# Optimization experiments

Hardware: AMD Instinct MI355X
Metric: run time of the kernel (lower is better)

## Reference

```python
import jax, jax.numpy as jnp
import numpy as np

N_NODES = 100000
N_EDGES = 1600000
IN_F = 128
OUT_F = 32


def setup_inputs() -> dict:
    key = jax.random.key(0)
    k1, k2, k3, k4, k5 = jax.random.split(key, 5)
    x = jax.random.normal(k1, (N_NODES, IN_F), dtype=jnp.float32)
    edge_row = jax.random.randint(k2, (N_EDGES,), 0, N_NODES, dtype=jnp.int64 if jax.config.jax_enable_x64 else jnp.int32)
    edge_col = jax.random.randint(k3, (N_EDGES,), 0, N_NODES, dtype=jnp.int64 if jax.config.jax_enable_x64 else jnp.int32)
    edge_val = jax.random.uniform(k4, (N_EDGES,), dtype=jnp.float32)
    # Xavier-normal init like nn.init.xavier_normal_
    std = float(np.sqrt(2.0 / (IN_F + OUT_F)))
    weight = jax.random.normal(k5, (IN_F, OUT_F), dtype=jnp.float32) * std
    bias = jnp.zeros((OUT_F,), dtype=jnp.float32)
    return {"x": x, "edge_row": edge_row, "edge_col": edge_col,
            "edge_val": edge_val, "weight": weight, "bias": bias}


def reference(x, edge_row, edge_col, edge_val, weight, bias):
    # support = x @ W  (dense GEMM)
    support = x @ weight  # [N, out]
    # output = adj @ support, adj in COO form: out[row] += val * support[col]
    gathered = support[edge_col] * edge_val[:, None]  # [E, out]
    output = jax.ops.segment_sum(gathered, edge_row, num_segments=N_NODES)
    return output + bias
```

## Files before the change

### kernel.cpp

```cpp
#include <hip/hip_runtime.h>
#include <hip/hip_bf16.h>

#define N_NODES 100000
#define N_EDGES 1600000
#define IN_F 128
#define OUT_F 32

#define NBK 782
#define CAP 2816
#define CAPG 2432
#define TILE_A 4096
#define NWG_A 391
#define NWG_G 98
#define OVCAP 4096

typedef float v4f __attribute__((ext_vector_type(4)));
typedef short bf16x8 __attribute__((ext_vector_type(8)));
typedef float f32x4 __attribute__((ext_vector_type(4)));

__device__ inline unsigned short f2bf(float f) {
  unsigned u = __float_as_uint(f);
  return (unsigned short)((u + 0x7FFFu + ((u >> 16) & 1u)) >> 16);
}
__device__ inline float bf2f(unsigned short h) {
  return __uint_as_float(((unsigned)h) << 16);
}
__device__ inline unsigned pk2(float lo, float hi) {
  return (unsigned)f2bf(lo) | ((unsigned)f2bf(hi) << 16);
}

__global__ __launch_bounds__(1024) void gcn_fused_kernel(
    const float* __restrict__ x, const float* __restrict__ w,
    unsigned short* __restrict__ sup, const int* __restrict__ erow,
    const int* __restrict__ ecol, const float* __restrict__ eval,
    int* __restrict__ cursor, int* __restrict__ ovcnt, int4* __restrict__ ov,
    int2* __restrict__ bedges) {
  __shared__ int2 stage[TILE_A];
  __shared__ int dstg[TILE_A];
  __shared__ int h[NBK];
  __shared__ int lstart[NBK];
  __shared__ int gbase[NBK];
  __shared__ int lcur[NBK];
  const int t = threadIdx.x;

  if (blockIdx.x < NWG_G) {
    const int wid = t >> 6;
    const int lane = t & 63;
    const int lr = lane & 15;
    const int lg = lane >> 4;
    const int wrow0 = blockIdx.x * 1024 + wid * 64;

    bf16x8 bfrag[2][4];
    #pragma unroll
    for (int nt = 0; nt < 2; ++nt) {
      #pragma unroll
      for (int kk = 0; kk < 4; ++kk) {
        const int c = nt * 16 + lr;
        const int k0 = kk * 32 + lg * 8;
        union { unsigned u[4]; bf16x8 v; } bf;
        #pragma unroll
        for (int d = 0; d < 4; ++d)
          bf.u[d] = pk2(w[(k0 + 2 * d) * OUT_F + c],
                        w[(k0 + 2 * d + 1) * OUT_F + c]);
        bfrag[nt][kk] = bf.v;
      }
    }

    f32x4 acc[4][2];
    #pragma unroll
    for (int m = 0; m < 4; ++m) { acc[m][0] = 0.f; acc[m][1] = 0.f; }

    #pragma unroll
    for (int m = 0; m < 4; ++m) {
      const int row = wrow0 + m * 16 + lr;
      const int rl = (row < N_NODES) ? row : (N_NODES - 1);
      const float* xr = x + (size_t)rl * IN_F;
      #pragma unroll
      for (int kk = 0; kk < 4; ++kk) {
        const v4f p0 = *(const v4f*)(xr + kk * 32 + lg * 8);
        const v4f p1 = *(const v4f*)(xr + kk * 32 + lg * 8 + 4);
        union { unsigned u[4]; bf16x8 v; } af;
        af.u[0] = pk2(p0.x, p0.y);
        af.u[1] = pk2(p0.z, p0.w);
        af.u[2] = pk2(p1.x, p1.y);
        af.u[3] = pk2(p1.z, p1.w);
        acc[m][0] = __builtin_amdgcn_mfma_f32_16x16x32_bf16(af.v, bfrag[0][kk], acc[m][0], 0, 0, 0);
        acc[m][1] = __builtin_amdgcn_mfma_f32_16x16x32_bf16(af.v, bfrag[1][kk], acc[m][1], 0, 0, 0);
      }
    }
    #pragma unroll
    for (int m = 0; m < 4; ++m) {
      #pragma unroll
      for (int i = 0; i < 4; ++i) {
        const int r = wrow0 + m * 16 + lg * 4 + i;
        if (r < N_NODES) {
          sup[((size_t)r << 5) + lr] = f2bf(acc[m][0][i]);
          sup[((size_t)r << 5) + 16 + lr] = f2bf(acc[m][1][i]);
        }
      }
    }
  } else {
    const int base = (blockIdx.x - NWG_G) * TILE_A;
    const int tot = min(TILE_A, N_EDGES - base);
    for (int i = t; i < NBK; i += 1024) { h[i] = 0; lcur[i] = 0; }
    __syncthreads();

    int rowv[4], colv[4];
    float valv[4];
    #pragma unroll
    for (int i = 0; i < 4; ++i) {
      const int e = base + i * 1024 + t;
      if (e < N_EDGES) {
        rowv[i] = erow[e]; colv[i] = ecol[e]; valv[i] = eval[e];
        atomicAdd(&h[rowv[i] >> 7], 1);
      } else rowv[i] = -1;
    }
    __syncthreads();

    if (t < 64) {
      const int b0 = t * 13;
      int vals[13];
      int s = 0;
      #pragma unroll
      for (int i = 0; i < 13; ++i) {
        const int b = b0 + i;
        vals[i] = (b < NBK) ? h[b] : 0;
        s += vals[i];
      }
      int ssum = s;
      #pragma unroll
      for (int off = 1; off < 64; off <<= 1) {
        const int up = __shfl_up(ssum, off, 64);
        if (t >= off) ssum += up;
      }
      int excl = ssum - s;
      #pragma unroll
      for (int i = 0; i < 13; ++i) {
        const int b = b0 + i;
        if (b < NBK) { lstart[b] = excl; excl += vals[i]; }
      }
    }
    if (t < NBK) {
      const int c = h[t];
      gbase[t] = c ? atomicAdd(&cursor[t], c) : 0;
    }
    __syncthreads();

    #pragma unroll
    for (int i = 0; i < 4; ++i) {
      if (rowv[i] >= 0) {
        const int r = rowv[i];
        const int b = r >> 7;
        const int k = atomicAdd(&lcur[b], 1);
        const int idx = lstart[b] + k;
        const int lo = colv[i] | ((r & 127) << 17);
        const int hi = __float_as_int(valv[i]);
        stage[idx] = make_int2(lo, hi);
        const int dst = gbase[b] + k;
        if (dst < CAP) {
          dstg[idx] = b * CAP + dst;
        } else {
          dstg[idx] = -1;
          const int o = atomicAdd(ovcnt, 1);
          if (o < OVCAP) ov[o] = make_int4(b, lo, hi, 0);
        }
      }
    }
    __syncthreads();

    for (int j = t; j < tot; j += 1024) {
      const int d = dstg[j];
      if (d >= 0) bedges[d] = stage[j];
    }
  }
}

__global__ __launch_bounds__(512) void gcn_gather_kernel(
    const unsigned short* __restrict__ sup, const int* __restrict__ cursor,
    const int2* __restrict__ bedges, const int* __restrict__ ovcnt,
    const int4* __restrict__ ov, const float* __restrict__ bias,
    float* __restrict__ out) {
  __shared__ int2 stage[CAPG];
  __shared__ int2 sorted[CAPG];
  __shared__ int hist[128];
  __shared__ int csr[129];
  __shared__ int cur[128];
  const int t = threadIdx.x;
  const int b = blockIdx.x;
  const int f = t & 31;
  const int g = t >> 5;
  const int ext = min(cursor[b], CAPG);
  const size_t bb = (size_t)b * CAP;
  float acc[8] = {0.f, 0.f, 0.f, 0.f, 0.f, 0.f, 0.f, 0.f};

  if (t < 128) hist[t] = 0;
  __syncthreads();
  for (int j = t; j < ext; j += 512) {
    const int2 ed = bedges[bb + j];
    stage[j] = ed;
    if (ed.y != 0) atomicAdd(&hist[(ed.x >> 17) & 127], 1);
  }
  __syncthreads();
  if (t < 64) {
    const int v0 = hist[2 * t];
    const int v1 = hist[2 * t + 1];
    int s = v0 + v1;
    #pragma unroll
    for (int off = 1; off < 64; off <<= 1) {
      const int up = __shfl_up(s, off, 64);
      if (t >= off) s += up;
    }
    const int excl = s - (v0 + v1);
    csr[2 * t] = excl;
    csr[2 * t + 1] = excl + v0;
    cur[2 * t] = excl;
    cur[2 * t + 1] = excl + v0;
    if (t == 63) csr[128] = s;
  }
  __syncthreads();
  for (int j = t; j < ext; j += 512) {
    const int2 ed = stage[j];
    if (ed.y != 0) {
      const int k = atomicAdd(&cur[(ed.x >> 17) & 127], 1);
      sorted[k] = ed;
    }
  }
  __syncthreads();

  #pragma unroll
  for (int rr = 0; rr < 8; ++rr) {
    const int lr = g * 8 + rr;
    const int e1 = csr[lr + 1];
    int e = csr[lr];
    for (; e + 8 <= e1; e += 8) {
      const int2 q0 = sorted[e],     q1 = sorted[e + 1];
      const int2 q2 = sorted[e + 2], q3 = sorted[e + 3];
      const int2 q4 = sorted[e + 4], q5 = sorted[e + 5];
      const int2 q6 = sorted[e + 6], q7 = sorted[e + 7];
      const float v0 = bf2f(sup[((size_t)(q0.x & 0x1FFFF) << 5) + f]);
      const float v1 = bf2f(sup[((size_t)(q1.x & 0x1FFFF) << 5) + f]);
      const float v2 = bf2f(sup[((size_t)(q2.x & 0x1FFFF) << 5) + f]);
      const float v3 = bf2f(sup[((size_t)(q3.x & 0x1FFFF) << 5) + f]);
      const float v4 = bf2f(sup[((size_t)(q4.x & 0x1FFFF) << 5) + f]);
      const float v5 = bf2f(sup[((size_t)(q5.x & 0x1FFFF) << 5) + f]);
      const float v6 = bf2f(sup[((size_t)(q6.x & 0x1FFFF) << 5) + f]);
      const float v7 = bf2f(sup[((size_t)(q7.x & 0x1FFFF) << 5) + f]);
      acc[rr] += __int_as_float(q0.y) * v0 + __int_as_float(q1.y) * v1 +
                 __int_as_float(q2.y) * v2 + __int_as_float(q3.y) * v3 +
                 __int_as_float(q4.y) * v4 + __int_as_float(q5.y) * v5 +
                 __int_as_float(q6.y) * v6 + __int_as_float(q7.y) * v7;
    }
    for (; e + 4 <= e1; e += 4) {
      const int2 q0 = sorted[e],     q1 = sorted[e + 1];
      const int2 q2 = sorted[e + 2], q3 = sorted[e + 3];
      const float v0 = bf2f(sup[((size_t)(q0.x & 0x1FFFF) << 5) + f]);
      const float v1 = bf2f(sup[((size_t)(q1.x & 0x1FFFF) << 5) + f]);
      const float v2 = bf2f(sup[((size_t)(q2.x & 0x1FFFF) << 5) + f]);
      const float v3 = bf2f(sup[((size_t)(q3.x & 0x1FFFF) << 5) + f]);
      acc[rr] += __int_as_float(q0.y) * v0 + __int_as_float(q1.y) * v1 +
                 __int_as_float(q2.y) * v2 + __int_as_float(q3.y) * v3;
    }
    for (; e < e1; ++e) {
      const int2 q = sorted[e];
      acc[rr] += __int_as_float(q.y) *
                 bf2f(sup[((size_t)(q.x & 0x1FFFF) << 5) + f]);
    }
  }

  const int on = min(*ovcnt, OVCAP);
  for (int i = 0; i < on; ++i) {
    const int4 q = ov[i];
    if (q.x == b) {
      const int lr = (q.y >> 17) & 127;
      if ((lr >> 3) == g)
        acc[lr & 7] += __int_as_float(q.z) *
                       bf2f(sup[((size_t)(q.y & 0x1FFFF) << 5) + f]);
    }
  }

  const int row0 = b << 7;
  const float bv = bias[f];
  #pragma unroll
  for (int rr = 0; rr < 8; ++rr) {
    const int row = row0 + g * 8 + rr;
    if (row < N_NODES) out[((size_t)row << 5) + f] = acc[rr] + bv;
  }
}

__global__ __launch_bounds__(256) void gcn_gemm_fb_kernel(
    const float* __restrict__ x, const float* __restrict__ w,
    unsigned short* __restrict__ sup) {
  __shared__ float wlds[IN_F][OUT_F];
  const int t = threadIdx.x;
  for (int i = t; i < 1024; i += 256)
    ((float4*)wlds)[i] = ((const float4*)w)[i];
  __syncthreads();
  const int tr = t >> 3;
  const int c0 = (t & 7) * 4;
  const int row = blockIdx.x * 32 + tr;
  if (row >= N_NODES) return;
  const float* xr = x + (size_t)row * IN_F;
  v4f acc = 0.f;
  #pragma unroll 4
  for (int kb = 0; kb < IN_F; kb += 4) {
    const v4f xv = *(const v4f*)(xr + kb);
    acc += xv.x * *(const v4f*)&wlds[kb + 0][c0];
    acc += xv.y * *(const v4f*)&wlds[kb + 1][c0];
    acc += xv.z * *(const v4f*)&wlds[kb + 2][c0];
    acc += xv.w * *(const v4f*)&wlds[kb + 3][c0];
  }
  ushort4 o;
  o.x = f2bf(acc.x); o.y = f2bf(acc.y); o.z = f2bf(acc.z); o.w = f2bf(acc.w);
  *(ushort4*)(sup + ((size_t)row << 5) + c0) = o;
}

__global__ __launch_bounds__(256) void gcn_init_out_kernel(
    float* __restrict__ out, const float* __restrict__ bias) {
  const int i = blockIdx.x * 256 + threadIdx.x;
  if (i < N_NODES * OUT_F / 4)
    ((float4*)out)[i] = ((const float4*)bias)[i & 7];
}

__global__ __launch_bounds__(256) void gcn_scatter_kernel(
    const unsigned short* __restrict__ sup, const int* __restrict__ erow,
    const int* __restrict__ ecol, const float* __restrict__ eval,
    float* __restrict__ out) {
  const long long idx = (long long)blockIdx.x * 256 + threadIdx.x;
  if (idx >= (long long)N_EDGES * OUT_F) return;
  const int e = (int)(idx >> 5);
  const int ff = (int)(idx & 31);
  atomicAdd(&out[((size_t)erow[e] << 5) + ff],
            eval[e] * bf2f(sup[((size_t)ecol[e] << 5) + ff]));
}

extern "C" void kernel_launch(void* const* d_in, const int* in_sizes, int n_in,
                              void* d_out, int out_size, void* d_ws, size_t ws_size,
                              hipStream_t stream) {
  const float* x = (const float*)d_in[0];
  const int* erow = (const int*)d_in[1];
  const int* ecol = (const int*)d_in[2];
  const float* eval = (const float*)d_in[3];
  const float* w = (const float*)d_in[4];
  const float* bias = (const float*)d_in[5];
  float* out = (float*)d_out;
  char* ws = (char*)d_ws;

  const size_t SUP_OFF = 0;
  const size_t CUR_OFF = SUP_OFF + 6400000;
  const size_t OVC_OFF = CUR_OFF + 3128;
  const size_t OV_OFF  = CUR_OFF + 3200;
  const size_t BED_OFF = OV_OFF + 65536;
  const size_t NEEDED  = BED_OFF + (size_t)NBK * CAP * 8;

  unsigned short* sup = (unsigned short*)(ws + SUP_OFF);

  if (ws_size >= NEEDED) {
    int* cursor = (int*)(ws + CUR_OFF);
    int* ovcnt  = (int*)(ws + OVC_OFF);
    int4* ov    = (int4*)(ws + OV_OFF);
    int2* bedges = (int2*)(ws + BED_OFF);

    hipMemsetAsync(cursor, 0, 3132, stream);
    gcn_fused_kernel<<<NWG_G + NWG_A, 1024, 0, stream>>>(
        x, w, sup, erow, ecol, eval, cursor, ovcnt, ov, bedges);
    gcn_gather_kernel<<<NBK, 512, 0, stream>>>(
        sup, cursor, bedges, ovcnt, ov, bias, out);
  } else if (ws_size >= 6400000) {
    gcn_gemm_fb_kernel<<<(N_NODES + 31) / 32, 256, 0, stream>>>(x, w, sup);
    gcn_init_out_kernel<<<(N_NODES * OUT_F / 4 + 255) / 256, 256, 0, stream>>>(out, bias);
    const long long total = (long long)N_EDGES * OUT_F;
    gcn_scatter_kernel<<<(int)((total + 255) / 256), 256, 0, stream>>>(
        sup, erow, ecol, eval, out);
  }
}
```

Before: 65.43 us.

## Split edge-binning tile into two sub-tiles with separate shared buffers

```diff
diff --git a/kernel.cpp b/kernel.cpp
--- a/kernel.cpp
+++ b/kernel.cpp
@@ -10,6 +10,7 @@
 #define CAP 2816
 #define CAPG 2432
 #define TILE_A 4096
+#define SUBT 2048
 #define NWG_A 391
 #define NWG_G 98
 #define OVCAP 4096
@@ -35,12 +36,12 @@
     const int* __restrict__ ecol, const float* __restrict__ eval,
     int* __restrict__ cursor, int* __restrict__ ovcnt, int4* __restrict__ ov,
     int2* __restrict__ bedges) {
-  __shared__ int2 stage[TILE_A];
-  __shared__ int dstg[TILE_A];
-  __shared__ int h[NBK];
-  __shared__ int lstart[NBK];
-  __shared__ int gbase[NBK];
-  __shared__ int lcur[NBK];
+  __shared__ int2 stage[2][SUBT];
+  __shared__ int dstg[2][SUBT];
+  __shared__ int h[2][NBK];
+  __shared__ int lstart[2][NBK];
+  __shared__ int gbase[2][NBK];
+  __shared__ int lcur[2][NBK];
   const int t = threadIdx.x;
 
   if (blockIdx.x < NWG_G) {
@@ -101,76 +102,79 @@
     }
   } else {
     const int base = (blockIdx.x - NWG_G) * TILE_A;
-    const int tot = min(TILE_A, N_EDGES - base);
-    for (int i = t; i < NBK; i += 1024) { h[i] = 0; lcur[i] = 0; }
-    __syncthreads();
-
-    int rowv[4], colv[4];
-    float valv[4];
-    #pragma unroll
-    for (int i = 0; i < 4; ++i) {
-      const int e = base + i * 1024 + t;
-      if (e < N_EDGES) {
-        rowv[i] = erow[e]; colv[i] = ecol[e]; valv[i] = eval[e];
-        atomicAdd(&h[rowv[i] >> 7], 1);
-      } else rowv[i] = -1;
-    }
-    __syncthreads();
-
-    if (t < 64) {
-      const int b0 = t * 13;
-      int vals[13];
-      int s = 0;
-      #pragma unroll
-      for (int i = 0; i < 13; ++i) {
-        const int b = b0 + i;
-        vals[i] = (b < NBK) ? h[b] : 0;
-        s += vals[i];
-      }
-      int ssum = s;
-      #pragma unroll
-      for (int off = 1; off < 64; off <<= 1) {
-        const int up = __shfl_up(ssum, off, 64);
-        if (t >= off) ssum += up;
-      }
-      int excl = ssum - s;
-      #pragma unroll
-      for (int i = 0; i < 13; ++i) {
-        const int b = b0 + i;
-        if (b < NBK) { lstart[b] = excl; excl += vals[i]; }
-      }
-    }
-    if (t < NBK) {
-      const int c = h[t];
-      gbase[t] = c ? atomicAdd(&cursor[t], c) : 0;
-    }
-    __syncthreads();
-
-    #pragma unroll
-    for (int i = 0; i < 4; ++i) {
-      if (rowv[i] >= 0) {
-        const int r = rowv[i];
-        const int b = r >> 7;
-        const int k = atomicAdd(&lcur[b], 1);
-        const int idx = lstart[b] + k;
-        const int lo = colv[i] | ((r & 127) << 17);
-        const int hi = __float_as_int(valv[i]);
-        stage[idx] = make_int2(lo, hi);
-        const int dst = gbase[b] + k;
-        if (dst < CAP) {
-          dstg[idx] = b * CAP + dst;
-        } else {
-          dstg[idx] = -1;
-          const int o = atomicAdd(ovcnt, 1);
-          if (o < OVCAP) ov[o] = make_int4(b, lo, hi, 0);
-        }
-      }
-    }
-    __syncthreads();
-
-    for (int j = t; j < tot; j += 1024) {
-      const int d = dstg[j];
-      if (d >= 0) bedges[d] = stage[j];
+    for (int s = 0; s < 2; ++s) {
+      const int sb = base + s * SUBT;
+      const int tot = min(SUBT, max(0, N_EDGES - sb));
+      for (int i = t; i < NBK; i += 1024) { h[s][i] = 0; lcur[s][i] = 0; }
+      __syncthreads();
+
+      int rowv[2], colv[2];
+      float valv[2];
+      #pragma unroll
+      for (int i = 0; i < 2; ++i) {
+        const int e = sb + i * 1024 + t;
+        if (e < N_EDGES && (i * 1024 + t) < tot) {
+          rowv[i] = erow[e]; colv[i] = ecol[e]; valv[i] = eval[e];
+          atomicAdd(&h[s][rowv[i] >> 7], 1);
+        } else rowv[i] = -1;
+      }
+      __syncthreads();
+
+      if (t < 64) {
+        const int b0 = t * 13;
+        int vals[13];
+        int sum = 0;
+        #pragma unroll
+        for (int i = 0; i < 13; ++i) {
+          const int b = b0 + i;
+          vals[i] = (b < NBK) ? h[s][b] : 0;
+          sum += vals[i];
+        }
+        int ssum = sum;
+        #pragma unroll
+        for (int off = 1; off < 64; off <<= 1) {
+          const int up = __shfl_up(ssum, off, 64);
+          if (t >= off) ssum += up;
+        }
+        int excl = ssum - sum;
+        #pragma unroll
+        for (int i = 0; i < 13; ++i) {
+          const int b = b0 + i;
+          if (b < NBK) { lstart[s][b] = excl; excl += vals[i]; }
+        }
+      }
+      if (t < NBK) {
+        const int c = h[s][t];
+        gbase[s][t] = c ? atomicAdd(&cursor[t], c) : 0;
+      }
+      __syncthreads();
+
+      #pragma unroll
+      for (int i = 0; i < 2; ++i) {
+        if (rowv[i] >= 0) {
+          const int r = rowv[i];
+          const int b = r >> 7;
+          const int k = atomicAdd(&lcur[s][b], 1);
+          const int idx = lstart[s][b] + k;
+          const int lo = colv[i] | ((r & 127) << 17);
+          const int hi = __float_as_int(valv[i]);
+          stage[s][idx] = make_int2(lo, hi);
+          const int dst = gbase[s][b] + k;
+          if (dst < CAP) {
+            dstg[s][idx] = b * CAP + dst;
+          } else {
+            dstg[s][idx] = -1;
+            const int o = atomicAdd(ovcnt, 1);
+            if (o < OVCAP) ov[o] = make_int4(b, lo, hi, 0);
+          }
+        }
+      }
+      __syncthreads();
+
+      for (int j = t; j < tot; j += 1024) {
+        const int d = dstg[s][j];
+        if (d >= 0) bedges[d] = stage[s][j];
+      }
     }
   }
 }
```

Result: slower. 67.05 us (+2.5%).

## Merge GEMM and edge-bucketing into uniform 512-thread workgroups

Applied to the files above, without the earlier changes.

```diff
diff --git a/kernel.cpp b/kernel.cpp
--- a/kernel.cpp
+++ b/kernel.cpp
@@ -9,9 +9,8 @@
 #define NBK 782
 #define CAP 2816
 #define CAPG 2432
-#define TILE_A 4096
-#define NWG_A 391
-#define NWG_G 98
+#define TILE_A 2048
+#define NWG 782
 #define OVCAP 4096
 
 typedef float v4f __attribute__((ext_vector_type(4)));
@@ -29,26 +28,38 @@
   return (unsigned)f2bf(lo) | ((unsigned)f2bf(hi) << 16);
 }
 
-__global__ __launch_bounds__(1024) void gcn_fused_kernel(
+__global__ __launch_bounds__(512, 8) void gcn_merged_kernel(
     const float* __restrict__ x, const float* __restrict__ w,
     unsigned short* __restrict__ sup, const int* __restrict__ erow,
     const int* __restrict__ ecol, const float* __restrict__ eval,
     int* __restrict__ cursor, int* __restrict__ ovcnt, int4* __restrict__ ov,
     int2* __restrict__ bedges) {
   __shared__ int2 stage[TILE_A];
-  __shared__ int dstg[TILE_A];
+  __shared__ unsigned short bof[TILE_A];
   __shared__ int h[NBK];
   __shared__ int lstart[NBK];
   __shared__ int gbase[NBK];
-  __shared__ int lcur[NBK];
   const int t = threadIdx.x;
-
-  if (blockIdx.x < NWG_G) {
+  const int base = blockIdx.x * TILE_A;
+  const int tot = min(TILE_A, N_EDGES - base);
+
+  int rowv[4], colv[4];
+  float valv[4];
+  #pragma unroll
+  for (int i = 0; i < 4; ++i) {
+    const int e = base + i * 512 + t;
+    if (e < N_EDGES) {
+      rowv[i] = erow[e]; colv[i] = ecol[e]; valv[i] = eval[e];
+    } else rowv[i] = -1;
+  }
+  for (int i = t; i < NBK; i += 512) h[i] = 0;
+
+  {
     const int wid = t >> 6;
     const int lane = t & 63;
     const int lr = lane & 15;
     const int lg = lane >> 4;
-    const int wrow0 = blockIdx.x * 1024 + wid * 64;
+    const int row0 = blockIdx.x * 128 + wid * 16;
 
     bf16x8 bfrag[2][4];
     #pragma unroll
@@ -66,111 +77,96 @@
       }
     }
 
-    f32x4 acc[4][2];
-    #pragma unroll
-    for (int m = 0; m < 4; ++m) { acc[m][0] = 0.f; acc[m][1] = 0.f; }
-
-    #pragma unroll
-    for (int m = 0; m < 4; ++m) {
-      const int row = wrow0 + m * 16 + lr;
-      const int rl = (row < N_NODES) ? row : (N_NODES - 1);
-      const float* xr = x + (size_t)rl * IN_F;
-      #pragma unroll
-      for (int kk = 0; kk < 4; ++kk) {
-        const v4f p0 = *(const v4f*)(xr + kk * 32 + lg * 8);
-        const v4f p1 = *(const v4f*)(xr + kk * 32 + lg * 8 + 4);
-        union { unsigned u[4]; bf16x8 v; } af;
-        af.u[0] = pk2(p0.x, p0.y);
-        af.u[1] = pk2(p0.z, p0.w);
-        af.u[2] = pk2(p1.x, p1.y);
-        af.u[3] = pk2(p1.z, p1.w);
-        acc[m][0] = __builtin_amdgcn_mfma_f32_16x16x32_bf16(af.v, bfrag[0][kk], acc[m][0], 0, 0, 0);
-        acc[m][1] = __builtin_amdgcn_mfma_f32_16x16x32_bf16(af.v, bfrag[1][kk], acc[m][1], 0, 0, 0);
+    f32x4 acc0 = {0.f, 0.f, 0.f, 0.f};
+    f32x4 acc1 = {0.f, 0.f, 0.f, 0.f};
+    const int row = row0 + lr;
+    const int rl = (row < N_NODES) ? row : (N_NODES - 1);
+    const float* xr = x + (size_t)rl * IN_F;
+    #pragma unroll
+    for (int kk = 0; kk < 4; ++kk) {
+      const v4f p0 = *(const v4f*)(xr + kk * 32 + lg * 8);
+      const v4f p1 = *(const v4f*)(xr + kk * 32 + lg * 8 + 4);
+      union { unsigned u[4]; bf16x8 v; } af;
+      af.u[0] = pk2(p0.x, p0.y);
+      af.u[1] = pk2(p0.z, p0.w);
+      af.u[2] = pk2(p1.x, p1.y);
+      af.u[3] = pk2(p1.z, p1.w);
+      acc0 = __builtin_amdgcn_mfma_f32_16x16x32_bf16(af.v, bfrag[0][kk], acc0, 0, 0, 0);
+      acc1 = __builtin_amdgcn_mfma_f32_16x16x32_bf16(af.v, bfrag[1][kk], acc1, 0, 0, 0);
+    }
+    #pragma unroll
+    for (int i = 0; i < 4; ++i) {
+      const int r = row0 + lg * 4 + i;
+      if (r < N_NODES) {
+        sup[((size_t)r << 5) + lr] = f2bf(acc0[i]);
+        sup[((size_t)r << 5) + 16 + lr] = f2bf(acc1[i]);
       }
     }
-    #pragma unroll
-    for (int m = 0; m < 4; ++m) {
-      #pragma unroll
-      for (int i = 0; i < 4; ++i) {
-        const int r = wrow0 + m * 16 + lg * 4 + i;
-        if (r < N_NODES) {
-          sup[((size_t)r << 5) + lr] = f2bf(acc[m][0][i]);
-          sup[((size_t)r << 5) + 16 + lr] = f2bf(acc[m][1][i]);
-        }
+  }
+  __syncthreads();
+
+  #pragma unroll
+  for (int i = 0; i < 4; ++i)
+    if (rowv[i] >= 0) atomicAdd(&h[rowv[i] >> 7], 1);
+  __syncthreads();
+
+  if (t < 64) {
+    const int b0 = t * 13;
+    int vals[13];
+    int sum = 0;
+    #pragma unroll
+    for (int i = 0; i < 13; ++i) {
+      const int b = b0 + i;
+      vals[i] = (b < NBK) ? h[b] : 0;
+      sum += vals[i];
+    }
+    int ssum = sum;
+    #pragma unroll
+    for (int off = 1; off < 64; off <<= 1) {
+      const int up = __shfl_up(ssum, off, 64);
+      if (t >= off) ssum += up;
+    }
+    int excl = ssum - sum;
+    #pragma unroll
+    for (int i = 0; i < 13; ++i) {
+      const int b = b0 + i;
+      if (b < NBK) { lstart[b] = excl; excl += vals[i]; }
+    }
+  }
+  __syncthreads();
+
+  for (int i = t; i < NBK; i += 512) {
+    const int c = h[i];
+    gbase[i] = c ? atomicAdd(&cursor[i], c) : 0;
+    h[i] = 0;
+  }
+  __syncthreads();
+
+  #pragma unroll
+  for (int i = 0; i < 4; ++i) {
+    if (rowv[i] >= 0) {
+      const int r = rowv[i];
+      const int b = r >> 7;
+      const int k = atomicAdd(&h[b], 1);
+      const int idx = lstart[b] + k;
+      stage[idx] = make_int2(colv[i] | ((r & 127) << 17),
+                             __float_as_int(valv[i]));
+      bof[idx] = (unsigned short)b;
+    }
+  }
+  __syncthreads();
+
+  for (int j = t; j < tot; j += 512) {
+    const int b = bof[j];
+    const int dst = gbase[b] + (j - lstart[b]);
+    if (dst >= 0 && dst < CAP) {
+      bedges[(size_t)b * CAP + dst] = stage[j];
+    } else {
+      const int o = atomicAdd(ovcnt, 1);
+      if (o < OVCAP) {
+        const int2 ed = stage[j];
+        ov[o] = make_int4(b, ed.x, ed.y, 0);
       }
-    }
-  } else {
-    const int base = (blockIdx.x - NWG_G) * TILE_A;
-    const int tot = min(TILE_A, N_EDGES - base);
-    for (int i = t; i < NBK; i += 1024) { h[i] = 0; lcur[i] = 0; }
-    __syncthreads();
-
-    int rowv[4], colv[4];
-    float valv[4];
-    #pragma unroll
-    for (int i = 0; i < 4; ++i) {
-      const int e = base + i * 1024 + t;
-      if (e < N_EDGES) {
-        rowv[i] = erow[e]; colv[i] = ecol[e]; valv[i] = eval[e];
-        atomicAdd(&h[rowv[i] >> 7], 1);
-      } else rowv[i] = -1;
-    }
-    __syncthreads();
-
-    if (t < 64) {
-      const int b0 = t * 13;
-      int vals[13];
-      int s = 0;
-      #pragma unroll
-      for (int i = 0; i < 13; ++i) {
-        const int b = b0 + i;
-        vals[i] = (b < NBK) ? h[b] : 0;
-        s += vals[i];
-      }
-      int ssum = s;
-      #pragma unroll
-      for (int off = 1; off < 64; off <<= 1) {
-        const int up = __shfl_up(ssum, off, 64);
-        if (t >= off) ssum += up;
-      }
-      int excl = ssum - s;
-      #pragma unroll
-      for (int i = 0; i < 13; ++i) {
-        const int b = b0 + i;
-        if (b < NBK) { lstart[b] = excl; excl += vals[i]; }
-      }
-    }
-    if (t < NBK) {
-      const int c = h[t];
-      gbase[t] = c ? atomicAdd(&cursor[t], c) : 0;
-    }
-    __syncthreads();
-
-    #pragma unroll
-    for (int i = 0; i < 4; ++i) {
-      if (rowv[i] >= 0) {
-        const int r = rowv[i];
-        const int b = r >> 7;
-        const int k = atomicAdd(&lcur[b], 1);
-        const int idx = lstart[b] + k;
-        const int lo = colv[i] | ((r & 127) << 17);
-        const int hi = __float_as_int(valv[i]);
-        stage[idx] = make_int2(lo, hi);
-        const int dst = gbase[b] + k;
-        if (dst < CAP) {
-          dstg[idx] = b * CAP + dst;
-        } else {
-          dstg[idx] = -1;
-          const int o = atomicAdd(ovcnt, 1);
-          if (o < OVCAP) ov[o] = make_int4(b, lo, hi, 0);
-        }
-      }
-    }
-    __syncthreads();
-
-    for (int j = t; j < tot; j += 1024) {
-      const int d = dstg[j];
-      if (d >= 0) bedges[d] = stage[j];
     }
   }
 }
@@ -198,7 +194,7 @@
   for (int j = t; j < ext; j += 512) {
     const int2 ed = bedges[bb + j];
     stage[j] = ed;
-    if (ed.y != 0) atomicAdd(&hist[(ed.x >> 17) & 127], 1);
+    atomicAdd(&hist[(ed.x >> 17) & 127], 1);
   }
   __syncthreads();
   if (t < 64) {
@@ -220,10 +216,8 @@
   __syncthreads();
   for (int j = t; j < ext; j += 512) {
     const int2 ed = stage[j];
-    if (ed.y != 0) {
-      const int k = atomicAdd(&cur[(ed.x >> 17) & 127], 1);
-      sorted[k] = ed;
-    }
+    const int k = atomicAdd(&cur[(ed.x >> 17) & 127], 1);
+    sorted[k] = ed;
   }
   __syncthreads();
 
@@ -361,7 +355,7 @@
     int2* bedges = (int2*)(ws + BED_OFF);
 
     hipMemsetAsync(cursor, 0, 3132, stream);
-    gcn_fused_kernel<<<NWG_G + NWG_A, 1024, 0, stream>>>(
+    gcn_merged_kernel<<<NWG, 512, 0, stream>>>(
         x, w, sup, erow, ecol, eval, cursor, ovcnt, ov, bedges);
     gcn_gather_kernel<<<NBK, 512, 0, stream>>>(
         sup, cursor, bedges, ovcnt, ov, bias, out);
```

Measured after the change: 80.44 us. 22.9% more time.
